# Performance work log

Hardware: AMD Instinct MI355X
Metric: run time of the kernel (lower is better)

Reference implementation:

```python
import jax, jax.numpy as jnp
import numpy as np

EMBED_DIM = 768
NUM_HEADS = 12
HEAD_DIM = EMBED_DIM // NUM_HEADS


def setup_inputs() -> dict:
    key = jax.random.key(0)
    ks = jax.random.split(key, 9)
    B, N, D = 1, 4096, EMBED_DIM
    s = 1.0 / np.sqrt(D)
    x = jax.random.normal(ks[0], (B, N, D), dtype=jnp.float32)
    Wq = jax.random.normal(ks[1], (D, D), dtype=jnp.float32) * s
    Wk = jax.random.normal(ks[2], (D, D), dtype=jnp.float32) * s
    Wv = jax.random.normal(ks[3], (D, D), dtype=jnp.float32) * s
    Wo = jax.random.normal(ks[4], (D, D), dtype=jnp.float32) * s
    bq = jax.random.normal(ks[5], (D,), dtype=jnp.float32) * 0.01
    bk = jax.random.normal(ks[6], (D,), dtype=jnp.float32) * 0.01
    bv = jax.random.normal(ks[7], (D,), dtype=jnp.float32) * 0.01
    bo = jax.random.normal(ks[8], (D,), dtype=jnp.float32) * 0.01
    return {"x": x, "Wq": Wq, "bq": bq, "Wk": Wk, "bk": bk,
            "Wv": Wv, "bv": bv, "Wo": Wo, "bo": bo}


def reference(x, Wq, bq, Wk, bk, Wv, bv, Wo, bo):
    B, N, D = x.shape
    h, d = NUM_HEADS, HEAD_DIM
    # projections; torch Linear computes x @ W.T + b, here W is stored as (in, out)
    q = (x @ Wq + bq).reshape(B, N, h, d).transpose(0, 2, 1, 3)  # [B,h,N,d]
    k = (x @ Wk + bk).reshape(B, N, h, d).transpose(0, 2, 1, 3)
    v = (x @ Wv + bv).reshape(B, N, h, d).transpose(0, 2, 1, 3)
    scores = jnp.einsum('bhnd,bhmd->bhnm', q, k) / np.sqrt(d)  # [B,h,N,N]
    attn = jax.nn.softmax(scores, axis=-1)
    out = jnp.einsum('bhnm,bhmd->bhnd', attn, v)  # [B,h,N,d]
    out = out.transpose(0, 2, 1, 3).reshape(B, N, D)
    return out @ Wo + bo
```

## Files before the change

### kernel.cpp

```cpp
#include <hip/hip_runtime.h>
#include <stdint.h>

#define EMBED 768
#define NTOK 4096
#define NHEAD 12
#define HD 64

typedef __attribute__((ext_vector_type(8))) short bf16x8;
typedef __attribute__((ext_vector_type(4))) float f32x4;
typedef __attribute__((ext_vector_type(16))) float f32x16;
typedef unsigned short ushort_t;

#define QSCALE 0.18033688011112042f

__device__ __forceinline__ unsigned short f2bf(float f) {
  union { float f; unsigned u; } c; c.f = f;
  unsigned u = c.u;
  u += 0x7fffu + ((u >> 16) & 1u);
  return (unsigned short)(u >> 16);
}

__device__ __forceinline__ void gld16(const void* g, void* l) {
  __builtin_amdgcn_global_load_lds((const __attribute__((address_space(1))) void*)g,
                                   (__attribute__((address_space(3))) void*)l,
                                   16, 0, 0);
}

__global__ void cvt_x_kernel(const float* __restrict__ x, ushort_t* __restrict__ xb) {
  size_t i = ((size_t)blockIdx.x * 256 + threadIdx.x) * 8;
  float4 a = *(const float4*)(x + i);
  float4 b = *(const float4*)(x + i + 4);
  uint4 p;
  p.x = (unsigned)f2bf(a.x) | ((unsigned)f2bf(a.y) << 16);
  p.y = (unsigned)f2bf(a.z) | ((unsigned)f2bf(a.w) << 16);
  p.z = (unsigned)f2bf(b.x) | ((unsigned)f2bf(b.y) << 16);
  p.w = (unsigned)f2bf(b.z) | ((unsigned)f2bf(b.w) << 16);
  *(uint4*)(xb + i) = p;
}

__global__ void transpose_w4_kernel(const float* __restrict__ w0, const float* __restrict__ w1,
                                    const float* __restrict__ w2, const float* __restrict__ w3,
                                    ushort_t* __restrict__ d0, ushort_t* __restrict__ d1,
                                    ushort_t* __restrict__ d2, ushort_t* __restrict__ d3) {
  __shared__ float t[32][33];
  int z = blockIdx.z;
  const float* w = (z == 0) ? w0 : (z == 1) ? w1 : (z == 2) ? w2 : w3;
  ushort_t* wt   = (z == 0) ? d0 : (z == 1) ? d1 : (z == 2) ? d2 : d3;
  int bx = blockIdx.x * 32, by = blockIdx.y * 32;
  int tx = threadIdx.x, ty = threadIdx.y;
  #pragma unroll
  for (int i = 0; i < 32; i += 8)
    t[ty + i][tx] = w[(size_t)(by + ty + i) * EMBED + bx + tx];
  __syncthreads();
  #pragma unroll
  for (int i = 0; i < 32; i += 8)
    wt[(size_t)(bx + ty + i) * EMBED + by + tx] = f2bf(t[tx][ty + i]);
}

template<int MODE>
__global__ __launch_bounds__(256)
void gemm_bt_kernel(const ushort_t* __restrict__ A, const ushort_t* __restrict__ Bt,
                    const float* __restrict__ b0, const float* __restrict__ b1,
                    const float* __restrict__ b2,
                    ushort_t* __restrict__ qo, ushort_t* __restrict__ ko,
                    ushort_t* __restrict__ vto, float* __restrict__ out) {
  __shared__ ushort_t As[128 * 32];
  __shared__ ushort_t Bs[128 * 32];
  const int K = EMBED;
  int tid = threadIdx.x, lane = tid & 63, wid = tid >> 6;
  int wy = wid >> 1, wx = wid & 1;
  int r0 = lane >> 4, cq = lane & 15;
  int brow = blockIdx.y * 128, bcol = blockIdx.x * 128;

  f32x4 acc[4][4] = {};

  for (int k0 = 0; k0 < K; k0 += 32) {
    #pragma unroll
    for (int c = 0; c < 2; ++c) {
      int chunk = wid * 2 + c;
      int eoff = chunk * 512;
      int le = eoff + lane * 8;
      int row = le >> 5, col = le & 31;
      gld16(A + (size_t)(brow + row) * K + k0 + col, As + eoff);
      gld16(Bt + (size_t)(bcol + row) * K + k0 + col, Bs + eoff);
    }
    __syncthreads();
    bf16x8 af[4], bfr[4];
    #pragma unroll
    for (int i = 0; i < 4; ++i)
      af[i] = *(const bf16x8*)(As + (wy * 64 + i * 16 + cq) * 32 + r0 * 8);
    #pragma unroll
    for (int i = 0; i < 4; ++i)
      bfr[i] = *(const bf16x8*)(Bs + (wx * 64 + i * 16 + cq) * 32 + r0 * 8);
    #pragma unroll
    for (int i = 0; i < 4; ++i)
      #pragma unroll
      for (int j = 0; j < 4; ++j)
        acc[i][j] = __builtin_amdgcn_mfma_f32_16x16x32_bf16(af[i], bfr[j], acc[i][j], 0, 0, 0);
    __syncthreads();
  }

  int sec = bcol / 768;
  int ncol0 = bcol - sec * 768;
  const float* bias = (sec == 0) ? b0 : (sec == 1) ? b1 : b2;
  #pragma unroll
  for (int i = 0; i < 4; ++i) {
    #pragma unroll
    for (int j = 0; j < 4; ++j) {
      #pragma unroll
      for (int jj = 0; jj < 4; ++jj) {
        int m = brow + wy * 64 + i * 16 + r0 * 4 + jj;
        int nn = ncol0 + wx * 64 + j * 16 + cq;
        float val = acc[i][j][jj] + bias[nn];
        if constexpr (MODE == 0) {
          int head = nn >> 6, dd = nn & 63;
          if (sec == 0)       qo[((size_t)head * NTOK + m) * HD + dd] = f2bf(val * QSCALE);
          else if (sec == 1)  ko[((size_t)head * NTOK + m) * HD + dd] = f2bf(val);
          else                vto[((size_t)head * HD + dd) * NTOK + m] = f2bf(val);
        } else {
          out[(size_t)m * EMBED + nn] = val;
        }
      }
    }
  }
}

__device__ __forceinline__ void stage_half(const ushort_t* kh, const ushort_t* vh,
                                           int kb, char* base, int srow, int sslot, int qg) {
  if (qg == 0) {
    const ushort_t* kg = kh + (size_t)kb * HD;
    #pragma unroll
    for (int i = 0; i < 8; ++i)
      gld16(kg + ((i * 8 + srow) * HD + sslot * 8), base + i * 1024);
  } else {
    const ushort_t* vg = vh + kb;
    char* vbuf = base + 8192;
    #pragma unroll
    for (int i = 0; i < 8; ++i)
      gld16(vg + ((size_t)(i * 8 + srow) * NTOK + sslot * 8), vbuf + i * 1024);
  }
}

__global__ __launch_bounds__(512, 2)
void flash_kernel(const ushort_t* __restrict__ q, const ushort_t* __restrict__ k,
                  const ushort_t* __restrict__ vt, ushort_t* __restrict__ o) {
  __shared__ __align__(16) char lds[131072];
  const int tid = threadIdx.x;
  const int lane = tid & 63;
  const int wid = tid >> 6;
  const int qg = wid >> 2;
  const int ks = wid & 3;
  const int head = blockIdx.y;
  const int qbase = blockIdx.x * 128 + qg * 64;
  const int c31 = lane & 31;
  const int hi = lane >> 5;
  const int l7 = lane & 7;
  const int srow = lane >> 3;
  const int sslot = (lane & 7) ^ srow;

  const ushort_t* qh = q + (size_t)head * NTOK * HD;
  const ushort_t* kh = k + (size_t)head * NTOK * HD;
  const ushort_t* vh = vt + (size_t)head * HD * NTOK;

  char* mybase = lds + ks * 32768;

  bf16x8 qf[2][4];
  #pragma unroll
  for (int qt = 0; qt < 2; ++qt)
    #pragma unroll
    for (int dc = 0; dc < 4; ++dc)
      qf[qt][dc] = *(const bf16x8*)(qh + (size_t)(qbase + qt * 32 + c31) * HD + dc * 16 + hi * 8);

  f32x16 oacc[2][2] = {};
  float lsum[2] = {0.f, 0.f};

  stage_half(kh, vh, ks * 64, mybase, srow, sslot, qg);

  #pragma unroll 2
  for (int it = 0; it < 16; ++it) {
    int cur = it & 1;
    __syncthreads();
    if (it < 15)
      stage_half(kh, vh, (ks + 4 * (it + 1)) * 64, mybase + (cur ^ 1) * 16384, srow, sslot, qg);
    const char* kbuf = mybase + cur * 16384;
    const char* vbuf = kbuf + 8192;

    f32x16 s[2][2] = {};
    #pragma unroll
    for (int dc = 0; dc < 4; ++dc)
      #pragma unroll
      for (int kt = 0; kt < 2; ++kt) {
        bf16x8 kf = *(const bf16x8*)(kbuf + (kt * 32 + c31) * 128 + (((dc * 2 + hi) ^ l7) * 16));
        #pragma unroll
        for (int qt = 0; qt < 2; ++qt)
          s[kt][qt] = __builtin_amdgcn_mfma_f32_32x32x16_bf16(kf, qf[qt][dc], s[kt][qt], 0, 0, 0);
      }

    union pfu { unsigned u[4]; bf16x8 v; };
    pfu pf[2][4];
    #pragma unroll
    for (int qt = 0; qt < 2; ++qt) {
      unsigned w[2][8];
      #pragma unroll
      for (int kt = 0; kt < 2; ++kt) {
        float p[16];
        #pragma unroll
        for (int r = 0; r < 16; ++r)
          p[r] = __builtin_amdgcn_exp2f(s[kt][qt][r]);
        float s4[4];
        #pragma unroll
        for (int g = 0; g < 4; ++g)
          s4[g] = (p[4 * g] + p[4 * g + 1]) + (p[4 * g + 2] + p[4 * g + 3]);
        lsum[qt] += (s4[0] + s4[1]) + (s4[2] + s4[3]);
        #pragma unroll
        for (int m = 0; m < 8; ++m)
          asm("v_cvt_pk_bf16_f32 %0, %1, %2" : "=v"(w[kt][m]) : "v"(p[2 * m]), "v"(p[2 * m + 1]));
      }
      #pragma unroll
      for (int kc = 0; kc < 4; ++kc) {
        int kt = kc >> 1, kl = kc & 1;
        #pragma unroll
        for (int e = 0; e < 2; ++e) {
          unsigned a = w[kt][e + 4 * kl];
          unsigned b = w[kt][e + 4 * kl + 2];
          asm("v_permlane32_swap_b32 %0, %1" : "+v"(a), "+v"(b));
          pf[qt][kc].u[e] = a;
          pf[qt][kc].u[e + 2] = b;
        }
      }
    }

    #pragma unroll
    for (int kc = 0; kc < 4; ++kc)
      #pragma unroll
      for (int dt = 0; dt < 2; ++dt) {
        bf16x8 vf = *(const bf16x8*)(vbuf + (dt * 32 + c31) * 128 + (((kc * 2 + hi) ^ l7) * 16));
        #pragma unroll
        for (int qt = 0; qt < 2; ++qt)
          oacc[dt][qt] = __builtin_amdgcn_mfma_f32_32x32x16_bf16(vf, pf[qt][kc].v, oacc[dt][qt], 0, 0, 0);
      }
  }

  __syncthreads();
  float* Oacc = (float*)lds;
  float* lacc = Oacc + 128 * 68;
  for (int t = tid; t < 128 * 68 + 128; t += 512)
    ((float*)lds)[t] = 0.f;
  __syncthreads();
  #pragma unroll
  for (int qt = 0; qt < 2; ++qt) {
    int qq = qg * 64 + qt * 32 + c31;
    atomicAdd(&lacc[qq], lsum[qt]);
    #pragma unroll
    for (int dt = 0; dt < 2; ++dt)
      #pragma unroll
      for (int g = 0; g < 4; ++g) {
        int dd = dt * 32 + 8 * g + 4 * hi;
        #pragma unroll
        for (int j = 0; j < 4; ++j)
          atomicAdd(&Oacc[qq * 68 + dd + j], oacc[dt][qt][4 * g + j]);
      }
  }
  __syncthreads();

  int qq = tid >> 2, seg = tid & 3;
  float linv = 1.0f / lacc[qq];
  unsigned outw[8];
  #pragma unroll
  for (int m = 0; m < 8; ++m) {
    float lo = Oacc[qq * 68 + seg * 16 + 2 * m] * linv;
    float hh = Oacc[qq * 68 + seg * 16 + 2 * m + 1] * linv;
    asm("v_cvt_pk_bf16_f32 %0, %1, %2" : "=v"(outw[m]) : "v"(lo), "v"(hh));
  }
  ushort_t* op = o + (size_t)(blockIdx.x * 128 + qq) * EMBED + head * HD + seg * 16;
  uint4 u0; u0.x = outw[0]; u0.y = outw[1]; u0.z = outw[2]; u0.w = outw[3];
  uint4 u1; u1.x = outw[4]; u1.y = outw[5]; u1.z = outw[6]; u1.w = outw[7];
  *(uint4*)op = u0;
  *((uint4*)op + 1) = u1;
}

extern "C" void kernel_launch(void* const* d_in, const int* in_sizes, int n_in,
                              void* d_out, int out_size, void* d_ws, size_t ws_size,
                              hipStream_t stream) {
  const float* x  = (const float*)d_in[0];
  const float* Wq = (const float*)d_in[1];
  const float* bq = (const float*)d_in[2];
  const float* Wk = (const float*)d_in[3];
  const float* bk = (const float*)d_in[4];
  const float* Wv = (const float*)d_in[5];
  const float* bv = (const float*)d_in[6];
  const float* Wo = (const float*)d_in[7];
  const float* bo = (const float*)d_in[8];
  float* out = (float*)d_out;

  char* ws = (char*)d_ws;
  ushort_t* xb    = (ushort_t*)ws;  ws += (size_t)NTOK * EMBED * 2;
  ushort_t* wqkvt = (ushort_t*)ws;  ws += (size_t)3 * EMBED * EMBED * 2;
  ushort_t* wot   = (ushort_t*)ws;  ws += (size_t)EMBED * EMBED * 2;
  ushort_t* qb    = (ushort_t*)ws;  ws += (size_t)NTOK * EMBED * 2;
  ushort_t* kb2   = (ushort_t*)ws;  ws += (size_t)NTOK * EMBED * 2;
  ushort_t* vtb   = (ushort_t*)ws;  ws += (size_t)NTOK * EMBED * 2;
  ushort_t* ao    = (ushort_t*)ws;  ws += (size_t)NTOK * EMBED * 2;

  cvt_x_kernel<<<(NTOK * EMBED) / (256 * 8), 256, 0, stream>>>(x, xb);
  transpose_w4_kernel<<<dim3(24, 24, 4), dim3(32, 8), 0, stream>>>(
      Wq, Wk, Wv, Wo,
      wqkvt, wqkvt + (size_t)EMBED * EMBED, wqkvt + (size_t)2 * EMBED * EMBED, wot);

  gemm_bt_kernel<0><<<dim3(2304 / 128, NTOK / 128), 256, 0, stream>>>(
      xb, wqkvt, bq, bk, bv, qb, kb2, vtb, nullptr);

  flash_kernel<<<dim3(NTOK / 128, NHEAD), 512, 0, stream>>>(qb, kb2, vtb, ao);

  gemm_bt_kernel<1><<<dim3(EMBED / 128, NTOK / 128), 256, 0, stream>>>(
      ao, wot, bo, nullptr, nullptr, nullptr, nullptr, nullptr, out);
}
```

Before: 292.5 us.

## Load K/V fragments directly from global into registers, drop LDS staging

```diff
diff --git a/kernel.cpp b/kernel.cpp
--- a/kernel.cpp
+++ b/kernel.cpp
@@ -125,45 +125,22 @@
   }
 }
 
-__device__ __forceinline__ void stage_half(const ushort_t* kh, const ushort_t* vh,
-                                           int kb, char* base, int srow, int sslot, int qg) {
-  if (qg == 0) {
-    const ushort_t* kg = kh + (size_t)kb * HD;
-    #pragma unroll
-    for (int i = 0; i < 8; ++i)
-      gld16(kg + ((i * 8 + srow) * HD + sslot * 8), base + i * 1024);
-  } else {
-    const ushort_t* vg = vh + kb;
-    char* vbuf = base + 8192;
-    #pragma unroll
-    for (int i = 0; i < 8; ++i)
-      gld16(vg + ((size_t)(i * 8 + srow) * NTOK + sslot * 8), vbuf + i * 1024);
-  }
-}
-
-__global__ __launch_bounds__(512, 2)
+__global__ __launch_bounds__(256, 2)
 void flash_kernel(const ushort_t* __restrict__ q, const ushort_t* __restrict__ k,
                   const ushort_t* __restrict__ vt, ushort_t* __restrict__ o) {
-  __shared__ __align__(16) char lds[131072];
+  __shared__ float cmb[64 * 68 + 64];
   const int tid = threadIdx.x;
   const int lane = tid & 63;
-  const int wid = tid >> 6;
-  const int qg = wid >> 2;
-  const int ks = wid & 3;
+  const int ks = tid >> 6;
   const int head = blockIdx.y;
-  const int qbase = blockIdx.x * 128 + qg * 64;
+  const int qbase = blockIdx.x * 64;
   const int c31 = lane & 31;
   const int hi = lane >> 5;
-  const int l7 = lane & 7;
-  const int srow = lane >> 3;
-  const int sslot = (lane & 7) ^ srow;
 
   const ushort_t* qh = q + (size_t)head * NTOK * HD;
   const ushort_t* kh = k + (size_t)head * NTOK * HD;
   const ushort_t* vh = vt + (size_t)head * HD * NTOK;
 
-  char* mybase = lds + ks * 32768;
-
   bf16x8 qf[2][4];
   #pragma unroll
   for (int qt = 0; qt < 2; ++qt)
@@ -174,27 +151,45 @@
   f32x16 oacc[2][2] = {};
   float lsum[2] = {0.f, 0.f};
 
-  stage_half(kh, vh, ks * 64, mybase, srow, sslot, qg);
-
-  #pragma unroll 2
+  bf16x8 kfr[8];
+  {
+    const ushort_t* kp = kh + (size_t)(ks * 64 + c31) * HD + hi * 8;
+    #pragma unroll
+    for (int kt = 0; kt < 2; ++kt)
+      #pragma unroll
+      for (int dc = 0; dc < 4; ++dc)
+        kfr[kt * 4 + dc] = *(const bf16x8*)(kp + kt * 32 * HD + dc * 16);
+  }
+
   for (int it = 0; it < 16; ++it) {
-    int cur = it & 1;
-    __syncthreads();
-    if (it < 15)
-      stage_half(kh, vh, (ks + 4 * (it + 1)) * 64, mybase + (cur ^ 1) * 16384, srow, sslot, qg);
-    const char* kbuf = mybase + cur * 16384;
-    const char* vbuf = kbuf + 8192;
+    const int kb = (ks + 4 * it) * 64;
 
     f32x16 s[2][2] = {};
+    __builtin_amdgcn_s_setprio(1);
     #pragma unroll
     for (int dc = 0; dc < 4; ++dc)
       #pragma unroll
-      for (int kt = 0; kt < 2; ++kt) {
-        bf16x8 kf = *(const bf16x8*)(kbuf + (kt * 32 + c31) * 128 + (((dc * 2 + hi) ^ l7) * 16));
+      for (int kt = 0; kt < 2; ++kt)
         #pragma unroll
         for (int qt = 0; qt < 2; ++qt)
-          s[kt][qt] = __builtin_amdgcn_mfma_f32_32x32x16_bf16(kf, qf[qt][dc], s[kt][qt], 0, 0, 0);
-      }
+          s[kt][qt] = __builtin_amdgcn_mfma_f32_32x32x16_bf16(kfr[kt * 4 + dc], qf[qt][dc], s[kt][qt], 0, 0, 0);
+    __builtin_amdgcn_s_setprio(0);
+
+    bf16x8 vfr[8];
+    #pragma unroll
+    for (int kc = 0; kc < 4; ++kc)
+      #pragma unroll
+      for (int dt = 0; dt < 2; ++dt)
+        vfr[kc * 2 + dt] = *(const bf16x8*)(vh + (size_t)(dt * 32 + c31) * NTOK + kb + kc * 16 + hi * 8);
+
+    if (it < 15) {
+      const ushort_t* kp = kh + (size_t)((ks + 4 * (it + 1)) * 64 + c31) * HD + hi * 8;
+      #pragma unroll
+      for (int kt = 0; kt < 2; ++kt)
+        #pragma unroll
+        for (int dc = 0; dc < 4; ++dc)
+          kfr[kt * 4 + dc] = *(const bf16x8*)(kp + kt * 32 * HD + dc * 16);
+    }
 
     union pfu { unsigned u[4]; bf16x8 v; };
     pfu pf[2][4];
@@ -230,26 +225,25 @@
       }
     }
 
+    __builtin_amdgcn_s_setprio(1);
     #pragma unroll
     for (int kc = 0; kc < 4; ++kc)
       #pragma unroll
-      for (int dt = 0; dt < 2; ++dt) {
-        bf16x8 vf = *(const bf16x8*)(vbuf + (dt * 32 + c31) * 128 + (((kc * 2 + hi) ^ l7) * 16));
+      for (int dt = 0; dt < 2; ++dt)
         #pragma unroll
         for (int qt = 0; qt < 2; ++qt)
-          oacc[dt][qt] = __builtin_amdgcn_mfma_f32_32x32x16_bf16(vf, pf[qt][kc].v, oacc[dt][qt], 0, 0, 0);
-      }
-  }
-
+          oacc[dt][qt] = __builtin_amdgcn_mfma_f32_32x32x16_bf16(vfr[kc * 2 + dt], pf[qt][kc].v, oacc[dt][qt], 0, 0, 0);
+    __builtin_amdgcn_s_setprio(0);
+  }
+
+  float* Oacc = cmb;
+  float* lacc = cmb + 64 * 68;
+  for (int t = tid; t < 64 * 68 + 64; t += 256)
+    cmb[t] = 0.f;
   __syncthreads();
-  float* Oacc = (float*)lds;
-  float* lacc = Oacc + 128 * 68;
-  for (int t = tid; t < 128 * 68 + 128; t += 512)
-    ((float*)lds)[t] = 0.f;
-  __syncthreads();
   #pragma unroll
   for (int qt = 0; qt < 2; ++qt) {
-    int qq = qg * 64 + qt * 32 + c31;
+    int qq = qt * 32 + c31;
     atomicAdd(&lacc[qq], lsum[qt]);
     #pragma unroll
     for (int dt = 0; dt < 2; ++dt)
@@ -272,7 +266,7 @@
     float hh = Oacc[qq * 68 + seg * 16 + 2 * m + 1] * linv;
     asm("v_cvt_pk_bf16_f32 %0, %1, %2" : "=v"(outw[m]) : "v"(lo), "v"(hh));
   }
-  ushort_t* op = o + (size_t)(blockIdx.x * 128 + qq) * EMBED + head * HD + seg * 16;
+  ushort_t* op = o + (size_t)(qbase + qq) * EMBED + head * HD + seg * 16;
   uint4 u0; u0.x = outw[0]; u0.y = outw[1]; u0.z = outw[2]; u0.w = outw[3];
   uint4 u1; u1.x = outw[4]; u1.y = outw[5]; u1.z = outw[6]; u1.w = outw[7];
   *(uint4*)op = u0;
@@ -310,7 +304,7 @@
   gemm_bt_kernel<0><<<dim3(2304 / 128, NTOK / 128), 256, 0, stream>>>(
       xb, wqkvt, bq, bk, bv, qb, kb2, vtb, nullptr);
 
-  flash_kernel<<<dim3(NTOK / 128, NHEAD), 512, 0, stream>>>(qb, kb2, vtb, ao);
+  flash_kernel<<<dim3(NTOK / 64, NHEAD), 256, 0, stream>>>(qb, kb2, vtb, ao);
 
   gemm_bt_kernel<1><<<dim3(EMBED / 128, NTOK / 128), 256, 0, stream>>>(
       ao, wot, bo, nullptr, nullptr, nullptr, nullptr, nullptr, out);
```

Measured after the change: 288.5 us. No clear change (-1.4%).
